# Kernel optimization log

Hardware: AMD Instinct MI355X
Metric: run time of the kernel (lower is better)

The kernel has to match this reference:

```python
import jax, jax.numpy as jnp
import numpy as np

B, L, D = 2048, 64, 512


def setup_inputs() -> dict:
    key = jax.random.key(0)
    ks = jax.random.split(key, 20)
    s = 1.0 / np.sqrt(D)
    inp = {
        "query_entity_encoding": jax.random.normal(ks[0], (B, L, D), jnp.float32),
        "relation_encoding": jax.random.normal(ks[1], (B, D), jnp.float32),
        "mask_emb": jax.random.normal(ks[2], (1, D), jnp.float32),
        "pos_e": jax.random.normal(ks[3], (100, D), jnp.float32),
        "pos_r": jax.random.normal(ks[4], (100, D), jnp.float32),
        "We_q": jax.random.normal(ks[5], (D, D), jnp.float32) * s,
        "be_q": jnp.zeros((D,), jnp.float32),
        "We_k": jax.random.normal(ks[6], (D, D), jnp.float32) * s,
        "be_k": jnp.zeros((D,), jnp.float32),
        "We_v": jax.random.normal(ks[7], (D, D), jnp.float32) * s,
        "be_v": jnp.zeros((D,), jnp.float32),
        "Wr_q": jax.random.normal(ks[8], (D, D), jnp.float32) * s,
        "br_q": jnp.zeros((D,), jnp.float32),
        "Wr_k": jax.random.normal(ks[9], (D, D), jnp.float32) * s,
        "br_k": jnp.zeros((D,), jnp.float32),
        "Wr_v": jax.random.normal(ks[10], (D, D), jnp.float32) * s,
        "br_v": jnp.zeros((D,), jnp.float32),
    }
    return inp


def _linear(x, W, b):
    # torch nn.Linear: y = x @ W.T + b
    return jnp.einsum("bld,ed->ble", x, W) + b


def reference(query_entity_encoding, relation_encoding, mask_emb, pos_e, pos_r,
              We_q, be_q, We_k, be_k, We_v, be_v,
              Wr_q, br_q, Wr_k, br_k, Wr_v, br_v):
    b, l, d = query_entity_encoding.shape  # l <= 99 assumed (matches init spec)
    # append mask token, add positional encodings
    mask_tok = jnp.broadcast_to(mask_emb[None, :, :], (b, 1, d))
    ent = jnp.concatenate([query_entity_encoding, mask_tok], axis=1)  # [b, l+1, d]
    ent = ent + pos_e[: l + 1][None, :, :]
    rel = relation_encoding[:, None, :] + pos_r[:l][None, :, :]  # [b, l, d]
    # six projections
    Qe, Ke, Ve = _linear(ent, We_q, be_q), _linear(ent, We_k, be_k), _linear(ent, We_v, be_v)
    Qr, Kr, Vr = _linear(rel, Wr_q, br_q), _linear(rel, Wr_k, br_k), _linear(rel, Wr_v, br_v)
    # block-concat attention == attention over concatenated streams
    Q = jnp.concatenate([Qe, Qr], axis=1)  # [b, 2l+1, d]
    K = jnp.concatenate([Ke, Kr], axis=1)
    V = jnp.concatenate([Ve, Vr], axis=1)
    scale = 1.0 / jnp.sqrt(jnp.asarray(d, Q.dtype))
    A = jnp.einsum("bqd,bkd->bqk", Q, K) * scale
    A = jax.nn.softmax(A, axis=-1)
    out = jnp.einsum("bqk,bkd->bqd", A, V)
    return out[:, 0]
```

## Files before the change

### kernel.cpp

```cpp
#include <hip/hip_runtime.h>
#include <math.h>


using s16x8 = __attribute__((ext_vector_type(8))) short;
using f32x4 = __attribute__((ext_vector_type(4))) float;

#define S12 1216

static __device__ __forceinline__ float bf2f(unsigned short s) {
  union { unsigned u; float f; } c; c.u = ((unsigned)s) << 16; return c.f;
}
static __device__ __forceinline__ unsigned short f2bf(float f) {
  union { float f; unsigned u; } c; c.f = f;
  unsigned u = c.u;
  unsigned r = (u + 0x7fffu + ((u >> 16) & 1u)) >> 16;
  return (unsigned short)r;
}

template <int K>
__device__ __forceinline__ void mfma64(
    const unsigned short* __restrict__ Ab, int lda,
    const unsigned short* __restrict__ Bb, int ldb,
    int wm, int wn, int lr, int koff, f32x4 acc[2][2]) {
#pragma unroll
  for (int k0 = 0; k0 < K; k0 += 32) {
    s16x8 a[2], b[2];
#pragma unroll
    for (int im = 0; im < 2; ++im)
      a[im] = *(const s16x8*)(Ab + (size_t)(wm + im * 16 + lr) * lda + k0 + koff);
#pragma unroll
    for (int in = 0; in < 2; ++in)
      b[in] = *(const s16x8*)(Bb + (size_t)(wn + in * 16 + lr) * ldb + k0 + koff);
#pragma unroll
    for (int im = 0; im < 2; ++im)
#pragma unroll
      for (int in = 0; in < 2; ++in)
        acc[im][in] = __builtin_amdgcn_mfma_f32_16x16x32_bf16(a[im], b[in], acc[im][in], 0, 0, 0);
  }
}

__global__ __launch_bounds__(256) void prep_kernel(
    const float* __restrict__ x, const float* __restrict__ rel,
    const float* __restrict__ pos_e, const float* __restrict__ pos_r,
    const float* __restrict__ maskv, const float* __restrict__ We_q,
    const float* __restrict__ We_k, const float* __restrict__ Wr_k,
    const float* __restrict__ We_v, const float* __restrict__ Wr_v,
    const float* __restrict__ be_k, const float* __restrict__ br_k,
    unsigned short* __restrict__ Xp, unsigned short* __restrict__ relb,
    unsigned short* __restrict__ Weqb, unsigned short* __restrict__ Wkb,
    unsigned short* __restrict__ WekT, unsigned short* __restrict__ Bt,
    unsigned short* __restrict__ Paug) {
  const int blk = blockIdx.x, tid = threadIdx.x;
  __shared__ float ts[64][65];
  if (blk < 2048) {
    float2 v = *(const float2*)(x + (size_t)blk * 32768 + tid * 2);
    float2 pe = *(const float2*)(pos_e + tid * 2);
    ushort2 o;
    o.x = f2bf(v.x + pe.x);
    o.y = f2bf(v.y + pe.y);
    *(ushort2*)(Xp + (size_t)blk * 512 + tid * 2) = o;
    float2 rv = *(const float2*)(rel + (size_t)blk * 512 + tid * 2);
    ushort2 ro;
    ro.x = f2bf(rv.x);
    ro.y = f2bf(rv.y);
    *(ushort2*)(relb + (size_t)blk * 512 + tid * 2) = ro;
  } else if (blk < 2176) {
    const int e = ((blk - 2048) * 256 + tid) * 8;
    float4 a0 = *(const float4*)(We_q + e);
    float4 a1 = *(const float4*)(We_q + e + 4);
    ushort4 o0, o1;
    o0.x = f2bf(a0.x); o0.y = f2bf(a0.y); o0.z = f2bf(a0.z); o0.w = f2bf(a0.w);
    o1.x = f2bf(a1.x); o1.y = f2bf(a1.y); o1.z = f2bf(a1.z); o1.w = f2bf(a1.w);
    *(ushort4*)(Weqb + e) = o0;
    *(ushort4*)(Weqb + e + 4) = o1;
  } else if (blk < 2432) {
    const int e = ((blk - 2176) * 256 + tid) * 8;
    const int n = e >> 10, k = e & 1023;
    const float* src = (k < 512) ? (We_k + (size_t)n * 512 + k)
                                 : (Wr_k + (size_t)n * 512 + k - 512);
    float4 v0 = *(const float4*)src;
    float4 v1 = *(const float4*)(src + 4);
    ushort4 o0, o1;
    o0.x = f2bf(v0.x); o0.y = f2bf(v0.y); o0.z = f2bf(v0.z); o0.w = f2bf(v0.w);
    o1.x = f2bf(v1.x); o1.y = f2bf(v1.y); o1.z = f2bf(v1.z); o1.w = f2bf(v1.w);
    *(ushort4*)(Wkb + e) = o0;
    *(ushort4*)(Wkb + e + 4) = o1;
  } else if (blk < 2496) {
    const int tr = blk - 2432;
    const int td0 = (tr >> 3) * 64, tn0 = (tr & 7) * 64;
    const int r = tid >> 2, cq = (tid & 3) * 16;
#pragma unroll
    for (int i = 0; i < 16; i += 4) {
      float4 v = *(const float4*)(We_k + (size_t)(tn0 + r) * 512 + td0 + cq + i);
      ts[r][cq + i + 0] = v.x;
      ts[r][cq + i + 1] = v.y;
      ts[r][cq + i + 2] = v.z;
      ts[r][cq + i + 3] = v.w;
    }
    __syncthreads();
#pragma unroll
    for (int i = 0; i < 16; i += 4) {
      ushort4 o;
      o.x = f2bf(ts[cq + i + 0][r]);
      o.y = f2bf(ts[cq + i + 1][r]);
      o.z = f2bf(ts[cq + i + 2][r]);
      o.w = f2bf(ts[cq + i + 3][r]);
      *(ushort4*)(WekT + (size_t)(td0 + r) * 512 + tn0 + cq + i) = o;
    }
  } else if (blk == 2496) {
    WekT[(size_t)512 * 512 + tid] = f2bf(be_k[tid]);
    WekT[(size_t)512 * 512 + 256 + tid] = f2bf(be_k[256 + tid]);
    WekT[(size_t)513 * 512 + tid] = f2bf(br_k[tid]);
    WekT[(size_t)513 * 512 + 256 + tid] = f2bf(br_k[256 + tid]);
  } else if (blk < 2513) {
    const int e = ((blk - 2497) * 256 + tid) * 8;
    if (e < 62 * 512) {
      ushort4 z = {0, 0, 0, 0};
      *(ushort4*)(WekT + (size_t)514 * 512 + e) = z;
      *(ushort4*)(WekT + (size_t)514 * 512 + e + 4) = z;
    }
  } else if (blk < 3025) {
    const int base = ((blk - 2513) * 256 + tid) * 4;
    const int n = base >> 10, k = base & 1023;
    const float* src = (k < 512) ? (We_v + (size_t)n * 512 + k)
                                 : (Wr_v + (size_t)n * 512 + k - 512);
    float4 v = *(const float4*)src;
    ushort4 o;
    o.x = f2bf(v.x); o.y = f2bf(v.y); o.z = f2bf(v.z); o.w = f2bf(v.w);
    *(ushort4*)(Bt + (size_t)n * S12 + k) = o;
  } else if (blk < 3041) {
    const int t = (blk - 3025) * 256 + tid;
    const int n = t >> 3, c0 = 1152 + (t & 7) * 8;
    ushort4 z = {0, 0, 0, 0};
    *(ushort4*)(Bt + (size_t)n * S12 + c0) = z;
    *(ushort4*)(Bt + (size_t)n * S12 + c0 + 4) = z;
  } else {
    const int idx = (blk - 3041) * 256 + tid;
    const int e = idx * 8;
    const int j = e >> 10, c = e & 1023;
    ushort4 o0 = {0, 0, 0, 0}, o1 = {0, 0, 0, 0};
    if (j < 65 && c < 512) {
      float4 v0 = *(const float4*)(pos_e + (size_t)j * 512 + c);
      float4 v1 = *(const float4*)(pos_e + (size_t)j * 512 + c + 4);
      if (j == 64) {
        float4 m0 = *(const float4*)(maskv + c);
        float4 m1 = *(const float4*)(maskv + c + 4);
        v0.x += m0.x; v0.y += m0.y; v0.z += m0.z; v0.w += m0.w;
        v1.x += m1.x; v1.y += m1.y; v1.z += m1.z; v1.w += m1.w;
      }
      o0.x = f2bf(v0.x); o0.y = f2bf(v0.y); o0.z = f2bf(v0.z); o0.w = f2bf(v0.w);
      o1.x = f2bf(v1.x); o1.y = f2bf(v1.y); o1.z = f2bf(v1.z); o1.w = f2bf(v1.w);
    } else if (j >= 65 && j < 129 && c >= 512) {
      float4 v0 = *(const float4*)(pos_r + (size_t)(j - 65) * 512 + c - 512);
      float4 v1 = *(const float4*)(pos_r + (size_t)(j - 65) * 512 + c - 512 + 4);
      o0.x = f2bf(v0.x); o0.y = f2bf(v0.y); o0.z = f2bf(v0.z); o0.w = f2bf(v0.w);
      o1.x = f2bf(v1.x); o1.y = f2bf(v1.y); o1.z = f2bf(v1.z); o1.w = f2bf(v1.w);
    }
    *(ushort4*)(Paug + e) = o0;
    *(ushort4*)(Paug + e + 4) = o1;
  }
}

__global__ __launch_bounds__(256) void g1_kernel(
    const unsigned short* __restrict__ Xp, const unsigned short* __restrict__ Weqb,
    const float* __restrict__ be_q, const unsigned short* __restrict__ relb,
    const unsigned short* __restrict__ Wkb, const unsigned short* __restrict__ Paug,
    unsigned short* __restrict__ Bt, unsigned short* __restrict__ qb,
    float* __restrict__ RW, unsigned short* __restrict__ GP) {
  int blk = blockIdx.x;
  const int tid = threadIdx.x;
  const int wid = tid >> 6, lane = tid & 63;
  const int wm = (wid >> 1) * 32, wn = (wid & 1) * 32;
  const int lr = lane & 15, koff = (lane >> 4) * 8;
  const int r0 = (lane >> 4) * 4;
  f32x4 acc[2][2] = {};
  if (blk < 256) {
    const int bm = (blk >> 3) * 64, bn = (blk & 7) * 64;
    mfma64<512>(Xp + (size_t)bm * 512, 512, Weqb + (size_t)bn * 512, 512,
                wm, wn, lr, koff, acc);
#pragma unroll
    for (int im = 0; im < 2; ++im)
#pragma unroll
      for (int in = 0; in < 2; ++in)
#pragma unroll
        for (int i = 0; i < 4; ++i) {
          const int row = bm + wm + im * 16 + r0 + i;
          const int col = bn + wn + in * 16 + lr;
          qb[(size_t)row * 512 + col] = f2bf(acc[im][in][i] + be_q[col]);
        }
  } else if (blk < 512) {
    blk -= 256;
    const int bm = (blk >> 3) * 64, bn = (blk & 7) * 64;
    mfma64<512>(relb + (size_t)bm * 512, 512, Wkb + (size_t)bn * 1024 + 512, 1024,
                wm, wn, lr, koff, acc);
#pragma unroll
    for (int im = 0; im < 2; ++im)
#pragma unroll
      for (int in = 0; in < 2; ++in)
#pragma unroll
        for (int i = 0; i < 4; ++i) {
          const int row = bm + wm + im * 16 + r0 + i;
          const int col = bn + wn + in * 16 + lr;
          RW[(size_t)row * 512 + col] = acc[im][in][i];
        }
  } else if (blk < 536) {
    blk -= 512;
    const int bm = (blk >> 3) * 64, bn = (blk & 7) * 64;
    mfma64<1024>(Paug + (size_t)bm * 1024, 1024, Wkb + (size_t)bn * 1024, 1024,
                 wm, wn, lr, koff, acc);
#pragma unroll
    for (int im = 0; im < 2; ++im)
#pragma unroll
      for (int in = 0; in < 2; ++in)
#pragma unroll
        for (int i = 0; i < 4; ++i) {
          const int row = bm + wm + im * 16 + r0 + i;
          const int col = bn + wn + in * 16 + lr;
          GP[(size_t)row * 512 + col] = f2bf(acc[im][in][i]);
        }
  } else {
    blk -= 536;
    const int bm = (blk >> 3) * 64, bn = (blk & 7) * 64;
    mfma64<1024>(Paug + (size_t)bm * 1024, 1024, Bt + (size_t)bn * S12, S12,
                 wm, wn, lr, koff, acc);
#pragma unroll
    for (int im = 0; im < 2; ++im)
#pragma unroll
      for (int in = 0; in < 2; ++in)
#pragma unroll
        for (int i = 0; i < 4; ++i) {
          const int row = bm + wm + im * 16 + r0 + i;
          const int col = bn + wn + in * 16 + lr;
          if (row < 129)
            Bt[(size_t)col * S12 + 1024 + row] = f2bf(acc[im][in][i]);
        }
  }
}

__global__ __launch_bounds__(256) void g2_kernel(
    const unsigned short* __restrict__ qb, const unsigned short* __restrict__ WekT,
    const unsigned short* __restrict__ GP, float* __restrict__ qke,
    float* __restrict__ sd) {
  int blk = blockIdx.x;
  const int tid = threadIdx.x;
  const int wid = tid >> 6, lane = tid & 63;
  const int wm = (wid >> 1) * 32, wn = (wid & 1) * 32;
  const int lr = lane & 15, koff = (lane >> 4) * 8;
  const int r0 = (lane >> 4) * 4;
  f32x4 acc[2][2] = {};
  if (blk < 288) {
    const int bm = (blk / 9) * 64, bn = (blk % 9) * 64;
    mfma64<512>(qb + (size_t)bm * 512, 512, WekT + (size_t)bn * 512, 512,
                wm, wn, lr, koff, acc);
#pragma unroll
    for (int im = 0; im < 2; ++im)
#pragma unroll
      for (int in = 0; in < 2; ++in)
#pragma unroll
        for (int i = 0; i < 4; ++i) {
          const int row = bm + wm + im * 16 + r0 + i;
          const int col = bn + wn + in * 16 + lr;
          qke[(size_t)row * 576 + col] = acc[im][in][i];
        }
  } else {
    blk -= 288;
    const int bm = (blk / 3) * 64, bn = (blk % 3) * 64;
    mfma64<512>(qb + (size_t)bm * 512, 512, GP + (size_t)bn * 512, 512,
                wm, wn, lr, koff, acc);
#pragma unroll
    for (int im = 0; im < 2; ++im)
#pragma unroll
      for (int in = 0; in < 2; ++in)
#pragma unroll
        for (int i = 0; i < 4; ++i) {
          const int row = bm + wm + im * 16 + r0 + i;
          const int col = bn + wn + in * 16 + lr;
          sd[(size_t)row * 192 + col] = acc[im][in][i];
        }
  }
}

__global__ __launch_bounds__(512, 4) void attn_kernel(
    const float* __restrict__ x, const float* __restrict__ rel,
    const float* __restrict__ qke, const float* __restrict__ sd,
    const unsigned short* __restrict__ qb, const float* __restrict__ RW,
    unsigned short* __restrict__ A, float* __restrict__ spe_g,
    float* __restrict__ spr_g) {
  __shared__ unsigned short xs[64 * 512];
  __shared__ unsigned short part[8 * 512];
  __shared__ float sdl[192];
  __shared__ float sc[64];
  __shared__ float pvv[129];
  __shared__ float scx[8];
  const int b = blockIdx.x;
  const int tid = threadIdx.x;
  const int wid = tid >> 6, lane = tid & 63;
  const int j0 = wid * 8;
  const float scale = 0.04419417382415922f;
  const float* xb = x + (size_t)b * 32768;

  if (tid < 192) sdl[tid] = sd[(size_t)b * 192 + tid];
  if (tid == 200) scx[1] = qke[(size_t)b * 576 + 512];
  float qe[8];
  {
    float4 a0 = *(const float4*)(qke + (size_t)b * 576 + lane * 8);
    float4 a1 = *(const float4*)(qke + (size_t)b * 576 + lane * 8 + 4);
    qe[0] = a0.x; qe[1] = a0.y; qe[2] = a0.z; qe[3] = a0.w;
    qe[4] = a1.x; qe[5] = a1.y; qe[6] = a1.z; qe[7] = a1.w;
  }

  {
    float a8[8];
#pragma unroll
    for (int r = 0; r < 8; ++r) {
      const int j = j0 + r;
      float4 v0 = *(const float4*)(xb + (size_t)j * 512 + lane * 8);
      float4 v1 = *(const float4*)(xb + (size_t)j * 512 + lane * 8 + 4);
      s16x8 u;
      u[0] = (short)f2bf(v0.x); u[1] = (short)f2bf(v0.y);
      u[2] = (short)f2bf(v0.z); u[3] = (short)f2bf(v0.w);
      u[4] = (short)f2bf(v1.x); u[5] = (short)f2bf(v1.y);
      u[6] = (short)f2bf(v1.z); u[7] = (short)f2bf(v1.w);
      *(s16x8*)(xs + (size_t)j * 512 + lane * 8) = u;
      a8[r] = qe[0] * v0.x + qe[1] * v0.y + qe[2] * v0.z + qe[3] * v0.w +
              qe[4] * v1.x + qe[5] * v1.y + qe[6] * v1.z + qe[7] * v1.w;
    }
#pragma unroll
    for (int off = 32; off > 0; off >>= 1) {
#pragma unroll
      for (int r = 0; r < 8; ++r) a8[r] += __shfl_xor(a8[r], off);
    }
    if (lane == 0) {
#pragma unroll
      for (int r = 0; r < 8; ++r) sc[j0 + r] = a8[r];
    }
  }
  if (wid == 7) {
    s16x8 qv = *(const s16x8*)(qb + (size_t)b * 512 + lane * 8);
    float4 r0 = *(const float4*)(RW + (size_t)b * 512 + lane * 8);
    float4 r1 = *(const float4*)(RW + (size_t)b * 512 + lane * 8 + 4);
    float s = bf2f(qv[0]) * r0.x + bf2f(qv[1]) * r0.y + bf2f(qv[2]) * r0.z +
              bf2f(qv[3]) * r0.w + bf2f(qv[4]) * r1.x + bf2f(qv[5]) * r1.y +
              bf2f(qv[6]) * r1.z + bf2f(qv[7]) * r1.w;
#pragma unroll
    for (int off = 32; off > 0; off >>= 1) s += __shfl_xor(s, off);
    if (lane == 0) scx[0] = s + qke[(size_t)b * 576 + 513];
  }
  __syncthreads();

  if (wid == 0) {
    const float crr = scx[0];
    const float qbk = scx[1];
    float v1 = (sc[lane] + sdl[lane] + qbk) * scale;
    float v2 = (lane == 0) ? (sdl[64] + qbk) * scale : (sdl[64 + lane] + crr) * scale;
    float v3 = (lane == 0) ? (sdl[128] + crr) * scale : -1e30f;
    float m = fmaxf(fmaxf(v1, v2), v3);
#pragma unroll
    for (int off = 32; off > 0; off >>= 1) m = fmaxf(m, __shfl_xor(m, off));
    float e1 = __expf(v1 - m);
    float e2 = __expf(v2 - m);
    float e3 = (lane == 0) ? __expf(v3 - m) : 0.f;
    float se = e1 + ((lane == 0) ? e2 : 0.f);
    float sr = ((lane == 0) ? 0.f : e2) + e3;
#pragma unroll
    for (int off = 32; off > 0; off >>= 1) {
      se += __shfl_xor(se, off);
      sr += __shfl_xor(sr, off);
    }
    float inv = 1.f / (se + sr);
    float p1 = e1 * inv, p2 = e2 * inv;
    pvv[lane] = p1;
    pvv[64 + lane] = p2;
    unsigned short* Ab = A + (size_t)b * S12;
    Ab[1024 + lane] = f2bf(p1);
    Ab[1088 + lane] = f2bf(p2);
    if (lane == 0) {
      float p3 = e3 * inv;
      pvv[128] = p3;
      Ab[1152] = f2bf(p3);
      scx[4] = sr * inv;
      spe_g[b] = se * inv;
      spr_g[b] = sr * inv;
    } else {
      Ab[1152 + lane] = 0;
    }
  }
  __syncthreads();

  {
    float acc8[8] = {};
#pragma unroll
    for (int r = 0; r < 8; ++r) {
      const float p = pvv[j0 + r];
      s16x8 xv = *(const s16x8*)(xs + (size_t)(j0 + r) * 512 + lane * 8);
      acc8[0] += p * bf2f(xv[0]); acc8[1] += p * bf2f(xv[1]);
      acc8[2] += p * bf2f(xv[2]); acc8[3] += p * bf2f(xv[3]);
      acc8[4] += p * bf2f(xv[4]); acc8[5] += p * bf2f(xv[5]);
      acc8[6] += p * bf2f(xv[6]); acc8[7] += p * bf2f(xv[7]);
    }
    s16x8 o;
#pragma unroll
    for (int i = 0; i < 8; ++i) o[i] = (short)f2bf(acc8[i]);
    *(s16x8*)(part + wid * 512 + lane * 8) = o;
  }
  __syncthreads();
  {
    float s = 0.f;
#pragma unroll
    for (int w = 0; w < 8; ++w) s += bf2f(part[w * 512 + tid]);
    unsigned short* Ab = A + (size_t)b * S12;
    Ab[tid] = f2bf(s);
    Ab[512 + tid] = f2bf(scx[4] * rel[(size_t)b * 512 + tid]);
  }
}

__global__ __launch_bounds__(256) void out_mfma_kernel(
    const unsigned short* __restrict__ A, const unsigned short* __restrict__ Bt,
    const float* __restrict__ be_v, const float* __restrict__ br_v,
    const float* __restrict__ spe, const float* __restrict__ spr,
    float* __restrict__ outp) {
  const int bn = blockIdx.x * 64;
  const int bm = blockIdx.y * 64;
  const int tid = threadIdx.x;
  const int wid = tid >> 6, lane = tid & 63;
  const int wm = (wid >> 1) * 32, wn = (wid & 1) * 32;
  const int lr = lane & 15, koff = (lane >> 4) * 8;
  f32x4 acc[2][2] = {};
  mfma64<S12>(A + (size_t)bm * S12, S12, Bt + (size_t)bn * S12, S12,
              wm, wn, lr, koff, acc);
  const int r0 = (lane >> 4) * 4;
#pragma unroll
  for (int im = 0; im < 2; ++im)
#pragma unroll
    for (int i = 0; i < 4; ++i) {
      const int row = bm + wm + im * 16 + r0 + i;
      const float se = spe[row], sr = spr[row];
#pragma unroll
      for (int in = 0; in < 2; ++in) {
        const int col = bn + wn + in * 16 + lr;
        outp[(size_t)row * 512 + col] = acc[im][in][i] + se * be_v[col] + sr * br_v[col];
      }
    }
}

extern "C" void kernel_launch(void* const* d_in, const int* in_sizes, int n_in,
                              void* d_out, int out_size, void* d_ws, size_t ws_size,
                              hipStream_t stream) {
  const float* x     = (const float*)d_in[0];
  const float* rel   = (const float*)d_in[1];
  const float* maskv = (const float*)d_in[2];
  const float* pos_e = (const float*)d_in[3];
  const float* pos_r = (const float*)d_in[4];
  const float* We_q  = (const float*)d_in[5];
  const float* be_q  = (const float*)d_in[6];
  const float* We_k  = (const float*)d_in[7];
  const float* be_k  = (const float*)d_in[8];
  const float* We_v  = (const float*)d_in[9];
  const float* be_v  = (const float*)d_in[10];
  const float* Wr_k  = (const float*)d_in[13];
  const float* br_k  = (const float*)d_in[14];
  const float* Wr_v  = (const float*)d_in[15];
  const float* br_v  = (const float*)d_in[16];

  char* p = (char*)d_ws;
  float* qke = (float*)p;                     p += (size_t)2048 * 576 * 4;
  float* sd  = (float*)p;                     p += (size_t)2048 * 192 * 4;
  float* RW  = (float*)p;                     p += (size_t)2048 * 512 * 4;
  float* spe = (float*)p;                     p += 2048 * 4;
  float* spr = (float*)p;                     p += 2048 * 4;
  unsigned short* qb   = (unsigned short*)p;  p += (size_t)2048 * 512 * 2;
  unsigned short* A    = (unsigned short*)p;  p += (size_t)2048 * S12 * 2;
  unsigned short* Bt   = (unsigned short*)p;  p += (size_t)512 * S12 * 2;
  unsigned short* WekT = (unsigned short*)p;  p += (size_t)576 * 512 * 2;
  unsigned short* Weqb = (unsigned short*)p;  p += (size_t)512 * 512 * 2;
  unsigned short* Wkb  = (unsigned short*)p;  p += (size_t)512 * 1024 * 2;
  unsigned short* GP   = (unsigned short*)p;  p += (size_t)192 * 512 * 2;
  unsigned short* Paug = (unsigned short*)p;  p += (size_t)192 * 1024 * 2;
  unsigned short* Xp   = (unsigned short*)p;  p += (size_t)2048 * 512 * 2;
  unsigned short* relb = (unsigned short*)p;  p += (size_t)2048 * 512 * 2;
  float* outp = (float*)d_out;

  prep_kernel<<<3137, 256, 0, stream>>>(x, rel, pos_e, pos_r, maskv, We_q,
                                        We_k, Wr_k, We_v, Wr_v, be_k, br_k,
                                        Xp, relb, Weqb, Wkb, WekT, Bt, Paug);
  g1_kernel<<<560, 256, 0, stream>>>(Xp, Weqb, be_q, relb, Wkb, Paug, Bt, qb,
                                     RW, GP);
  g2_kernel<<<384, 256, 0, stream>>>(qb, WekT, GP, qke, sd);
  attn_kernel<<<2048, 512, 0, stream>>>(x, rel, qke, sd, qb, RW, A, spe, spr);
  out_mfma_kernel<<<dim3(8, 32), 256, 0, stream>>>(A, Bt, be_v, br_v, spe, spr,
                                                   outp);
}
```

Baseline: 131.0 us.

## Stream entity rows through double-buffered LDS via global_load_lds in attention kernel

Replaces the direct per-wave global float4 loads of the 64x512 entity tile with a double-buffered pipeline that uses global_load_lds into a 2x8x512 fp32 staging buffer. Each batch of eight rows is converted to bf16 and dotted with the query as soon as it lands, while the next batch is in flight. Rows are now interleaved across waves (row i*8+wid) instead of contiguous blocks. The extra 32KB of LDS and the lowered launch bounds reduce occupancy from several blocks per CU to likely one, and the per-batch barriers add synchronisation.

```diff
diff --git a/kernel.cpp b/kernel.cpp
--- a/kernel.cpp
+++ b/kernel.cpp
@@ -280,12 +280,13 @@
   }
 }
 
-__global__ __launch_bounds__(512, 4) void attn_kernel(
+__global__ __launch_bounds__(512, 1) void attn_kernel(
     const float* __restrict__ x, const float* __restrict__ rel,
     const float* __restrict__ qke, const float* __restrict__ sd,
     const unsigned short* __restrict__ qb, const float* __restrict__ RW,
     unsigned short* __restrict__ A, float* __restrict__ spe_g,
     float* __restrict__ spr_g) {
+  __shared__ float stage[2][8 * 512];
   __shared__ unsigned short xs[64 * 512];
   __shared__ unsigned short part[8 * 512];
   __shared__ float sdl[192];
@@ -308,33 +309,6 @@
     qe[0] = a0.x; qe[1] = a0.y; qe[2] = a0.z; qe[3] = a0.w;
     qe[4] = a1.x; qe[5] = a1.y; qe[6] = a1.z; qe[7] = a1.w;
   }
-
-  {
-    float a8[8];
-#pragma unroll
-    for (int r = 0; r < 8; ++r) {
-      const int j = j0 + r;
-      float4 v0 = *(const float4*)(xb + (size_t)j * 512 + lane * 8);
-      float4 v1 = *(const float4*)(xb + (size_t)j * 512 + lane * 8 + 4);
-      s16x8 u;
-      u[0] = (short)f2bf(v0.x); u[1] = (short)f2bf(v0.y);
-      u[2] = (short)f2bf(v0.z); u[3] = (short)f2bf(v0.w);
-      u[4] = (short)f2bf(v1.x); u[5] = (short)f2bf(v1.y);
-      u[6] = (short)f2bf(v1.z); u[7] = (short)f2bf(v1.w);
-      *(s16x8*)(xs + (size_t)j * 512 + lane * 8) = u;
-      a8[r] = qe[0] * v0.x + qe[1] * v0.y + qe[2] * v0.z + qe[3] * v0.w +
-              qe[4] * v1.x + qe[5] * v1.y + qe[6] * v1.z + qe[7] * v1.w;
-    }
-#pragma unroll
-    for (int off = 32; off > 0; off >>= 1) {
-#pragma unroll
-      for (int r = 0; r < 8; ++r) a8[r] += __shfl_xor(a8[r], off);
-    }
-    if (lane == 0) {
-#pragma unroll
-      for (int r = 0; r < 8; ++r) sc[j0 + r] = a8[r];
-    }
-  }
   if (wid == 7) {
     s16x8 qv = *(const s16x8*)(qb + (size_t)b * 512 + lane * 8);
     float4 r0 = *(const float4*)(RW + (size_t)b * 512 + lane * 8);
@@ -345,6 +319,65 @@
 #pragma unroll
     for (int off = 32; off > 0; off >>= 1) s += __shfl_xor(s, off);
     if (lane == 0) scx[0] = s + qke[(size_t)b * 576 + 513];
+  }
+
+  float a8[8];
+#pragma unroll
+  for (int r = 0; r < 8; ++r) a8[r] = 0.f;
+
+  __builtin_amdgcn_sched_barrier(0);
+  asm volatile("s_waitcnt vmcnt(0)" ::: "memory");
+  __builtin_amdgcn_sched_barrier(0);
+
+#define ISSUE_BATCH(i)                                                        \
+  {                                                                           \
+    const float* gsrc = xb + (i) * 4096 + wid * 512;                          \
+    float* ldst = &stage[(i) & 1][wid * 512];                                 \
+    __builtin_amdgcn_global_load_lds(                                         \
+        (const __attribute__((address_space(1))) void*)(gsrc + lane * 4),     \
+        (__attribute__((address_space(3))) void*)(ldst), 16, 0, 0);           \
+    __builtin_amdgcn_global_load_lds(                                         \
+        (const __attribute__((address_space(1))) void*)(gsrc + 256 + lane * 4),\
+        (__attribute__((address_space(3))) void*)(ldst + 256), 16, 0, 0);     \
+  }
+
+  ISSUE_BATCH(0);
+#pragma unroll
+  for (int i = 0; i < 8; ++i) {
+    if (i < 7) ISSUE_BATCH(i + 1);
+    if (i < 7)
+      asm volatile("s_waitcnt vmcnt(2)" ::: "memory");
+    else
+      asm volatile("s_waitcnt vmcnt(0)" ::: "memory");
+    __builtin_amdgcn_sched_barrier(0);
+    __builtin_amdgcn_s_barrier();
+    {
+      const float* srow = &stage[i & 1][wid * 512];
+      float4 v0 = *(const float4*)(srow + lane * 8);
+      float4 v1 = *(const float4*)(srow + lane * 8 + 4);
+      const int j = i * 8 + wid;
+      s16x8 u;
+      u[0] = (short)f2bf(v0.x); u[1] = (short)f2bf(v0.y);
+      u[2] = (short)f2bf(v0.z); u[3] = (short)f2bf(v0.w);
+      u[4] = (short)f2bf(v1.x); u[5] = (short)f2bf(v1.y);
+      u[6] = (short)f2bf(v1.z); u[7] = (short)f2bf(v1.w);
+      *(s16x8*)(xs + (size_t)j * 512 + lane * 8) = u;
+      a8[i] = qe[0] * v0.x + qe[1] * v0.y + qe[2] * v0.z + qe[3] * v0.w +
+              qe[4] * v1.x + qe[5] * v1.y + qe[6] * v1.z + qe[7] * v1.w;
+    }
+    __builtin_amdgcn_s_barrier();
+    __builtin_amdgcn_sched_barrier(0);
+  }
+#undef ISSUE_BATCH
+
+#pragma unroll
+  for (int off = 32; off > 0; off >>= 1) {
+#pragma unroll
+    for (int r = 0; r < 8; ++r) a8[r] += __shfl_xor(a8[r], off);
+  }
+  if (lane == 0) {
+#pragma unroll
+    for (int r = 0; r < 8; ++r) sc[r * 8 + wid] = a8[r];
   }
   __syncthreads();
 
```

After: 155.5 us. 18.7% more time.
